# Kernel optimization log

Measured on AMD Instinct MI355X. Metric: run time of the kernel, lower is better.

## Reference

```python
import jax, jax.numpy as jnp
import numpy as np

B, S, IN, H, O, K = 64, 256, 512, 1024, 512, 4


def setup_inputs() -> dict:
    key = jax.random.key(0)
    ks = jax.random.split(key, 8)
    s = 1.0 / np.sqrt(H)  # torch RNNCell/Linear default uniform init bound
    return {
        "x_seq": jax.random.normal(ks[0], (B, S, IN), jnp.float32),
        "y_seq": jax.random.randint(ks[1], (B, S), 0, O, dtype=jnp.int64),
        "seq_mask": jnp.ones((B, S, 1), jnp.float32),
        "forced_num_ticks": K,
        "W_ih": jax.random.uniform(ks[2], (3 * H, IN), jnp.float32, -s, s),
        "W_hh": jax.random.uniform(ks[3], (3 * H, H), jnp.float32, -s, s),
        "b_ih": jax.random.uniform(ks[4], (3 * H,), jnp.float32, -s, s),
        "b_hh": jax.random.uniform(ks[5], (3 * H,), jnp.float32, -s, s),
        "W_fc": jax.random.uniform(ks[6], (O, H), jnp.float32, -s, s),
        "b_fc": jax.random.uniform(ks[7], (O,), jnp.float32, -s, s),
    }


def gru_cell(x, h, W_ih, W_hh, b_ih, b_hh):
    # torch.nn.GRUCell math
    gi = x @ W_ih.T + b_ih  # [B, 3H]
    gh = h @ W_hh.T + b_hh  # [B, 3H]
    i_r, i_z, i_n = jnp.split(gi, 3, axis=-1)
    h_r, h_z, h_n = jnp.split(gh, 3, axis=-1)
    r = jax.nn.sigmoid(i_r + h_r)
    z = jax.nn.sigmoid(i_z + h_z)
    n = jnp.tanh(i_n + r * h_n)
    return (1.0 - z) * n + z * h


def reference(x_seq, y_seq, seq_mask, forced_num_ticks, W_ih, W_hh, b_ih, b_hh, W_fc, b_fc):
    k = int(forced_num_ticks)
    b = x_seq.shape[0]
    # With forced_num_ticks=k, the inner while-loop runs exactly k ticks per
    # timestep for every sample; the same x_t / seq_mask[:,t,:] are reused
    # for all k ticks, and hidden state persists across timesteps.
    xs = jnp.repeat(x_seq, k, axis=1).transpose(1, 0, 2)      # [S*k, B, IN]
    sms = jnp.repeat(seq_mask, k, axis=1).transpose(1, 0, 2)  # [S*k, B, 1]
    h0 = jnp.zeros((b, W_hh.shape[1]), x_seq.dtype)

    def step(h, inp):
        x_t, sm_t = inp
        h_new = gru_cell(x_t, h, W_ih, W_hh, b_ih, b_hh)
        logits_t = (h_new @ W_fc.T + b_fc) * sm_t  # mask = not_finished * sm_t (not_finished always True)
        return h_new, logits_t

    _, logits = jax.lax.scan(step, h0, (xs, sms))  # logits: [S*k, B, O]
    logits_seq = logits.transpose(1, 0, 2)         # [B, S*k, O]
    y_res = jnp.repeat(y_seq, k, axis=1)           # [B, S*k]
    ok = jnp.repeat(seq_mask[:, :, 0] != 0, k, axis=1)  # [B, S*k] bool (mask_last=True)
    return logits_seq, y_res, ok
```

## Files before the change

### kernel.cpp

```cpp
#include <hip/hip_runtime.h>
#include <hip/hip_bf16.h>

#define B_ 64
#define S_ 256
#define IN_ 512
#define H_ 1024
#define O_ 512
#define K_ 4
#define T_ (S_*K_)
#define H3_ (3*H_)

#define NC_ 8
#define CPC_ 32
#define RPC_ 8

typedef __attribute__((ext_vector_type(8))) short bf16x8;
typedef __attribute__((ext_vector_type(4))) float f32x4;
typedef __attribute__((ext_vector_type(4))) unsigned int uint32x4;
typedef unsigned short ushort_t;
typedef unsigned int uint_t;
typedef unsigned long long ull_t;

__device__ __forceinline__ ushort_t f2b(float f) {
    union { float f; unsigned u; } v; v.f = f;
    unsigned r = v.u + 0x7FFFu + ((v.u >> 16) & 1u);
    return (ushort_t)(r >> 16);
}
__device__ __forceinline__ float b2f(ushort_t h) {
    union { unsigned u; float f; } v; v.u = ((unsigned)h) << 16; return v.f;
}

__global__ __launch_bounds__(256) void gi_gemm(const float* __restrict__ x,
                                               const float* __restrict__ Wih,
                                               const float* __restrict__ bih,
                                               ushort_t* __restrict__ gi) {
    const int NB = H3_ / 64;
    const int nb = blockIdx.x % NB;
    const int mb = blockIdx.x / NB;
    const int tid = threadIdx.x, lane = tid & 63, w = tid >> 6;
    const int wm = w >> 1, wn = w & 1;
    __shared__ ushort_t Al[64][40];
    __shared__ ushort_t Bl[64][40];
    f32x4 acc[2][2] = {};
    const int lrow = tid >> 2, lk = (tid & 3) * 8;
    for (int k0 = 0; k0 < IN_; k0 += 32) {
        const float* xs = &x[(size_t)(mb*64 + lrow)*IN_ + k0 + lk];
        const float* ws = &Wih[(size_t)(nb*64 + lrow)*IN_ + k0 + lk];
        #pragma unroll
        for (int i = 0; i < 8; ++i) Al[lrow][lk+i] = f2b(xs[i]);
        #pragma unroll
        for (int i = 0; i < 8; ++i) Bl[lrow][lk+i] = f2b(ws[i]);
        __syncthreads();
        const int fr = lane & 15, fk = (lane >> 4) * 8;
        #pragma unroll
        for (int mt = 0; mt < 2; ++mt) {
            bf16x8 a = *(const bf16x8*)&Al[wm*32 + mt*16 + fr][fk];
            #pragma unroll
            for (int nt = 0; nt < 2; ++nt) {
                bf16x8 b = *(const bf16x8*)&Bl[wn*32 + nt*16 + fr][fk];
                acc[mt][nt] = __builtin_amdgcn_mfma_f32_16x16x32_bf16(a, b, acc[mt][nt], 0, 0, 0);
            }
        }
        __syncthreads();
    }
    const int fr = lane & 15, fm = (lane >> 4) * 4;
    #pragma unroll
    for (int mt = 0; mt < 2; ++mt)
    #pragma unroll
    for (int nt = 0; nt < 2; ++nt)
    #pragma unroll
    for (int i = 0; i < 4; ++i) {
        int gm = mb*64 + wm*32 + mt*16 + fm + i;
        int gn = nb*64 + wn*32 + nt*16 + fr;
        gi[(size_t)gm*H3_ + gn] = f2b(acc[mt][nt][i] + bih[gn]);
    }
}

__global__ __launch_bounds__(256) void rec_kernel(const ushort_t* __restrict__ gi,
                                                  const float* __restrict__ Whh,
                                                  const float* __restrict__ bhh,
                                                  ushort_t* __restrict__ hstates,
                                                  ushort_t* __restrict__ xbuf,
                                                  int* __restrict__ flags) {
    const int bid = blockIdx.x;
    const int c  = bid & 7;
    const int cu = bid >> 3;
    const int tid = threadIdx.x, lane = tid & 63, w = tid >> 6;
    const int r_el = tid >> 5, jl = tid & 31;
    const int fr = lane & 15, koff8 = (lane >> 4) << 3;
    const int colbase = cu << 5;
    const int b0 = c * RPC_;

    __shared__ ushort_t wlds[48][1032];
    __shared__ float red[4][8][100];

    for (int e = tid * 4; e < 48 * 1024; e += 256 * 4) {
        int rr = e >> 10, k = e & 1023;
        int wrow = (rr < 32) ? (colbase + rr) : (H_ + colbase + (rr - 32));
        const float* src = &Whh[(size_t)wrow*H_ + k];
        #pragma unroll
        for (int i = 0; i < 4; ++i) wlds[rr][k + i] = f2b(src[i]);
    }
    bf16x8 bz1[8], bn0[8], bn1[8];
    #pragma unroll
    for (int ks = 0; ks < 8; ++ks) {
        const int kk = (w << 8) + (ks << 5) + koff8;
        const float* sz = &Whh[(size_t)(H_   + colbase + 16 + fr)*H_ + kk];
        const float* s0 = &Whh[(size_t)(2*H_ + colbase      + fr)*H_ + kk];
        const float* s1 = &Whh[(size_t)(2*H_ + colbase + 16 + fr)*H_ + kk];
        bf16x8 tz, t0, t1;
        #pragma unroll
        for (int i = 0; i < 8; ++i) {
            tz[i] = (short)f2b(sz[i]); t0[i] = (short)f2b(s0[i]); t1[i] = (short)f2b(s1[i]);
        }
        bz1[ks] = tz; bn0[ks] = t0; bn1[ks] = t1;
    }
    const float bh_r = bhh[colbase + jl];
    const float bh_z = bhh[H_ + colbase + jl];
    const float bh_n = bhh[2*H_ + colbase + jl];

    ushort_t g_r, g_z, g_n, p_r = 0, p_z = 0, p_n = 0;
    {
        size_t row = ((size_t)(b0 + r_el)*S_ + 0)*H3_ + colbase + jl;
        g_r = gi[row]; g_z = gi[row + H_]; g_n = gi[row + 2*H_];
    }
    float gir = 0.f, giz = 0.f, gin = 0.f;

    const char* xb_lane = (const char*)xbuf
        + ((size_t)c << 16)
        + (size_t)fr * 2048
        + (w << 9)
        + ((lane >> 4) << 4);

    float h_prev = 0.f;
    int* cflags = &flags[c << 5];
    __syncthreads();

    for (int t = 0; t < T_; ++t) {
        if ((t & 3) == 0) {
            if (t > 0) { g_r = p_r; g_z = p_z; g_n = p_n; }
            gir = b2f(g_r); giz = b2f(g_z); gin = b2f(g_n);
            int sn = (t >> 2) + 1; if (sn > S_ - 1) sn = S_ - 1;
            size_t row = ((size_t)(b0 + r_el)*S_ + sn)*H3_ + colbase + jl;
            p_r = gi[row]; p_z = gi[row + H_]; p_n = gi[row + 2*H_];
        }

        uint32x4 f0 = {}, f1 = {}, f2 = {}, f3 = {}, f4 = {}, f5 = {}, f6 = {}, f7 = {};
        if (t > 0) {
            const char* ab = xb_lane + (((size_t)((t - 1) & 1)) << 15);
            asm volatile(
                "global_load_dwordx4 %0, %8, off sc0 sc1\n\t"
                "global_load_dwordx4 %1, %8, off offset:64 sc0 sc1\n\t"
                "global_load_dwordx4 %2, %8, off offset:128 sc0 sc1\n\t"
                "global_load_dwordx4 %3, %8, off offset:192 sc0 sc1\n\t"
                "global_load_dwordx4 %4, %8, off offset:256 sc0 sc1\n\t"
                "global_load_dwordx4 %5, %8, off offset:320 sc0 sc1\n\t"
                "global_load_dwordx4 %6, %8, off offset:384 sc0 sc1\n\t"
                "global_load_dwordx4 %7, %8, off offset:448 sc0 sc1\n\t"
                "s_waitcnt vmcnt(0)"
                : "=&v"(f0), "=&v"(f1), "=&v"(f2), "=&v"(f3),
                  "=&v"(f4), "=&v"(f5), "=&v"(f6), "=&v"(f7)
                : "v"(ab)
                : "memory");
            __builtin_amdgcn_sched_barrier(0);
        }
        bf16x8 afr[8];
        afr[0] = *(bf16x8*)&f0; afr[1] = *(bf16x8*)&f1;
        afr[2] = *(bf16x8*)&f2; afr[3] = *(bf16x8*)&f3;
        afr[4] = *(bf16x8*)&f4; afr[5] = *(bf16x8*)&f5;
        afr[6] = *(bf16x8*)&f6; afr[7] = *(bf16x8*)&f7;

        f32x4 ar0 = {}, ar1 = {}, az0 = {}, az1 = {}, an0 = {}, an1 = {};
        #pragma unroll
        for (int ks = 0; ks < 8; ++ks) {
            const int k = (w << 8) + (ks << 5) + koff8;
            bf16x8 br0 = *(const bf16x8*)&wlds[fr][k];
            bf16x8 br1 = *(const bf16x8*)&wlds[16 + fr][k];
            bf16x8 bz0 = *(const bf16x8*)&wlds[32 + fr][k];
            ar0 = __builtin_amdgcn_mfma_f32_16x16x32_bf16(afr[ks], br0, ar0, 0, 0, 0);
            ar1 = __builtin_amdgcn_mfma_f32_16x16x32_bf16(afr[ks], br1, ar1, 0, 0, 0);
            az0 = __builtin_amdgcn_mfma_f32_16x16x32_bf16(afr[ks], bz0, az0, 0, 0, 0);
            az1 = __builtin_amdgcn_mfma_f32_16x16x32_bf16(afr[ks], bz1[ks], az1, 0, 0, 0);
            an0 = __builtin_amdgcn_mfma_f32_16x16x32_bf16(afr[ks], bn0[ks], an0, 0, 0, 0);
            an1 = __builtin_amdgcn_mfma_f32_16x16x32_bf16(afr[ks], bn1[ks], an1, 0, 0, 0);
        }
        if (lane < 32) {
            const int m = (lane >> 4) << 2, n = fr;
            #pragma unroll
            for (int i = 0; i < 4; ++i) {
                red[w][m+i][n]      = ar0[i];
                red[w][m+i][16+n]   = ar1[i];
                red[w][m+i][32+n]   = az0[i];
                red[w][m+i][48+n]   = az1[i];
                red[w][m+i][64+n]   = an0[i];
                red[w][m+i][80+n]   = an1[i];
            }
        }
        __syncthreads();

        float ghr = red[0][r_el][jl]    + red[1][r_el][jl]    + red[2][r_el][jl]    + red[3][r_el][jl];
        float ghz = red[0][r_el][32+jl] + red[1][r_el][32+jl] + red[2][r_el][32+jl] + red[3][r_el][32+jl];
        float ghn = red[0][r_el][64+jl] + red[1][r_el][64+jl] + red[2][r_el][64+jl] + red[3][r_el][64+jl];
        float rr_ = 1.f / (1.f + __expf(-(gir + ghr + bh_r)));
        float zz  = 1.f / (1.f + __expf(-(giz + ghz + bh_z)));
        float nn  = tanhf(gin + rr_ * (ghn + bh_n));
        float hn  = (1.f - zz) * nn + zz * h_prev;
        h_prev = hn;
        ushort_t hb = f2b(hn);

        hstates[((size_t)(b0 + r_el)*T_ + t)*H_ + colbase + jl] = hb;
        size_t xidx = ((size_t)c << 15) + ((size_t)(t & 1) << 14) + (r_el << 10) + colbase + jl;
        __hip_atomic_store(&xbuf[xidx], hb, __ATOMIC_RELAXED, __HIP_MEMORY_SCOPE_AGENT);

        __syncthreads();

        if (w == 0) {
            if (lane == 0)
                __hip_atomic_store(&cflags[cu], t + 1, __ATOMIC_RELAXED,
                                   __HIP_MEMORY_SCOPE_AGENT);
            for (;;) {
                int v = t + 1;
                if (lane < 32)
                    v = __hip_atomic_load(&cflags[lane], __ATOMIC_RELAXED,
                                          __HIP_MEMORY_SCOPE_AGENT);
                if (__all(v >= t + 1)) break;
                __builtin_amdgcn_s_sleep(1);
            }
        }
        __syncthreads();
    }
}

__global__ __launch_bounds__(256) void logits_gemm(const ushort_t* __restrict__ hstates,
                                                   const float* __restrict__ Wfc,
                                                   const float* __restrict__ bfc,
                                                   const float* __restrict__ sm,
                                                   float* __restrict__ out) {
    const int NB = O_ / 64;
    const int nb = blockIdx.x % NB;
    const int mb = blockIdx.x / NB;
    const int tid = threadIdx.x, lane = tid & 63, w = tid >> 6;
    const int wm = w >> 1, wn = w & 1;
    __shared__ ushort_t Al[64][40];
    __shared__ ushort_t Bl[64][40];
    f32x4 acc[2][2] = {};
    const int lrow = tid >> 2, lk = (tid & 3) * 8;
    for (int k0 = 0; k0 < H_; k0 += 32) {
        uint4 va = *(const uint4*)&hstates[(size_t)(mb*64 + lrow)*H_ + k0 + lk];
        *(uint4*)&Al[lrow][lk] = va;
        const float* ws = &Wfc[(size_t)(nb*64 + lrow)*H_ + k0 + lk];
        #pragma unroll
        for (int i = 0; i < 8; ++i) Bl[lrow][lk+i] = f2b(ws[i]);
        __syncthreads();
        const int fr = lane & 15, fk = (lane >> 4) * 8;
        #pragma unroll
        for (int mt = 0; mt < 2; ++mt) {
            bf16x8 a = *(const bf16x8*)&Al[wm*32 + mt*16 + fr][fk];
            #pragma unroll
            for (int nt = 0; nt < 2; ++nt) {
                bf16x8 b = *(const bf16x8*)&Bl[wn*32 + nt*16 + fr][fk];
                acc[mt][nt] = __builtin_amdgcn_mfma_f32_16x16x32_bf16(a, b, acc[mt][nt], 0, 0, 0);
            }
        }
        __syncthreads();
    }
    const int fr = lane & 15, fm = (lane >> 4) * 4;
    #pragma unroll
    for (int mt = 0; mt < 2; ++mt)
    #pragma unroll
    for (int nt = 0; nt < 2; ++nt)
    #pragma unroll
    for (int i = 0; i < 4; ++i) {
        int R  = mb*64 + wm*32 + mt*16 + fm + i;
        int gn = nb*64 + wn*32 + nt*16 + fr;
        int b  = R >> 10, t = R & (T_ - 1);
        float mval = sm[b*S_ + (t >> 2)];
        out[(size_t)R*O_ + gn] = (acc[mt][nt][i] + bfc[gn]) * mval;
    }
}

__global__ void tail_kernel(const int* __restrict__ y, const float* __restrict__ sm,
                            float* __restrict__ yout, float* __restrict__ okout) {
    int i = blockIdx.x * 256 + threadIdx.x;
    if (i < B_ * T_) {
        int b = i >> 10, t = i & 1023, s = t >> 2;
        yout[i]  = (float)y[b*S_ + s];
        okout[i] = (sm[b*S_ + s] != 0.0f) ? 1.0f : 0.0f;
    }
}

extern "C" void kernel_launch(void* const* d_in, const int* in_sizes, int n_in,
                              void* d_out, int out_size, void* d_ws, size_t ws_size,
                              hipStream_t stream) {
    (void)in_sizes; (void)n_in; (void)out_size; (void)ws_size;
    const float* x   = (const float*)d_in[0];
    const int*   y   = (const int*)d_in[1];
    const float* sm  = (const float*)d_in[2];
    const float* Wih = (const float*)d_in[4];
    const float* Whh = (const float*)d_in[5];
    const float* bih = (const float*)d_in[6];
    const float* bhh = (const float*)d_in[7];
    const float* Wfc = (const float*)d_in[8];
    const float* bfc = (const float*)d_in[9];

    char* ws = (char*)d_ws;
    ushort_t* gi      = (ushort_t*)ws;
    ushort_t* hstates = (ushort_t*)(ws + 100663296);
    ushort_t* xbuf    = (ushort_t*)(ws + 100663296 + 134217728);
    int*      flags   = (int*)(ws + 100663296 + 134217728 + 524288);

    hipMemsetAsync(flags, 0, 4096, stream);

    hipLaunchKernelGGL(gi_gemm, dim3((B_*S_/64)*(H3_/64)), dim3(256), 0, stream,
                       x, Wih, bih, gi);

    void* args[] = { (void*)&gi, (void*)&Whh, (void*)&bhh, (void*)&hstates,
                     (void*)&xbuf, (void*)&flags };
    hipLaunchCooperativeKernel((void*)rec_kernel, dim3(NC_*CPC_), dim3(256), args, 0, stream);

    hipLaunchKernelGGL(logits_gemm, dim3((B_*T_/64)*(O_/64)), dim3(256), 0, stream,
                       hstates, Wfc, bfc, sm, (float*)d_out);

    float* yout  = (float*)d_out + (size_t)B_*T_*O_;
    float* okout = yout + (size_t)B_*T_;
    hipLaunchKernelGGL(tail_kernel, dim3(B_*T_/256), dim3(256), 0, stream,
                       y, sm, yout, okout);
}
```

Baseline: 3.655 ms.

## Replace flag barrier with step-tagged hidden-state words polled directly

```diff
diff --git a/kernel.cpp b/kernel.cpp
--- a/kernel.cpp
+++ b/kernel.cpp
@@ -19,7 +19,6 @@
 typedef __attribute__((ext_vector_type(4))) unsigned int uint32x4;
 typedef unsigned short ushort_t;
 typedef unsigned int uint_t;
-typedef unsigned long long ull_t;
 
 __device__ __forceinline__ ushort_t f2b(float f) {
     union { float f; unsigned u; } v; v.f = f;
@@ -80,8 +79,7 @@
                                                   const float* __restrict__ Whh,
                                                   const float* __restrict__ bhh,
                                                   ushort_t* __restrict__ hstates,
-                                                  ushort_t* __restrict__ xbuf,
-                                                  int* __restrict__ flags) {
+                                                  uint_t* __restrict__ xbuf) {
     const int bid = blockIdx.x;
     const int c  = bid & 7;
     const int cu = bid >> 3;
@@ -92,7 +90,7 @@
     const int b0 = c * RPC_;
 
     __shared__ ushort_t wlds[48][1032];
-    __shared__ float red[4][8][100];
+    __shared__ float red[2][4][8][100];
 
     for (int e = tid * 4; e < 48 * 1024; e += 256 * 4) {
         int rr = e >> 10, k = e & 1023;
@@ -127,48 +125,74 @@
     float gir = 0.f, giz = 0.f, gin = 0.f;
 
     const char* xb_lane = (const char*)xbuf
-        + ((size_t)c << 16)
-        + (size_t)fr * 2048
-        + (w << 9)
-        + ((lane >> 4) << 4);
+        + ((size_t)c << 17)
+        + (size_t)fr * 4096
+        + (w << 10)
+        + ((lane >> 4) << 5);
 
     float h_prev = 0.f;
-    int* cflags = &flags[c << 5];
     __syncthreads();
 
     for (int t = 0; t < T_; ++t) {
         if ((t & 3) == 0) {
             if (t > 0) { g_r = p_r; g_z = p_z; g_n = p_n; }
             gir = b2f(g_r); giz = b2f(g_z); gin = b2f(g_n);
-            int sn = (t >> 2) + 1; if (sn > S_ - 1) sn = S_ - 1;
-            size_t row = ((size_t)(b0 + r_el)*S_ + sn)*H3_ + colbase + jl;
-            p_r = gi[row]; p_z = gi[row + H_]; p_n = gi[row + 2*H_];
-        }
-
-        uint32x4 f0 = {}, f1 = {}, f2 = {}, f3 = {}, f4 = {}, f5 = {}, f6 = {}, f7 = {};
+        }
+
+        uint32x4 f0={},f1={},f2={},f3={},f4={},f5={},f6={},f7={};
+        uint32x4 f8={},f9={},f10={},f11={},f12={},f13={},f14={},f15={};
         if (t > 0) {
-            const char* ab = xb_lane + (((size_t)((t - 1) & 1)) << 15);
-            asm volatile(
-                "global_load_dwordx4 %0, %8, off sc0 sc1\n\t"
-                "global_load_dwordx4 %1, %8, off offset:64 sc0 sc1\n\t"
-                "global_load_dwordx4 %2, %8, off offset:128 sc0 sc1\n\t"
-                "global_load_dwordx4 %3, %8, off offset:192 sc0 sc1\n\t"
-                "global_load_dwordx4 %4, %8, off offset:256 sc0 sc1\n\t"
-                "global_load_dwordx4 %5, %8, off offset:320 sc0 sc1\n\t"
-                "global_load_dwordx4 %6, %8, off offset:384 sc0 sc1\n\t"
-                "global_load_dwordx4 %7, %8, off offset:448 sc0 sc1\n\t"
-                "s_waitcnt vmcnt(0)"
-                : "=&v"(f0), "=&v"(f1), "=&v"(f2), "=&v"(f3),
-                  "=&v"(f4), "=&v"(f5), "=&v"(f6), "=&v"(f7)
-                : "v"(ab)
-                : "memory");
+            const char* ab = xb_lane + (((size_t)((t - 1) & 1)) << 16);
+            const uint_t tagw = ((uint_t)(t - 1)) << 16;
+            for (;;) {
+                asm volatile(
+                    "global_load_dwordx4 %0, %16, off sc0 sc1\n\t"
+                    "global_load_dwordx4 %1, %16, off offset:16 sc0 sc1\n\t"
+                    "global_load_dwordx4 %2, %16, off offset:128 sc0 sc1\n\t"
+                    "global_load_dwordx4 %3, %16, off offset:144 sc0 sc1\n\t"
+                    "global_load_dwordx4 %4, %16, off offset:256 sc0 sc1\n\t"
+                    "global_load_dwordx4 %5, %16, off offset:272 sc0 sc1\n\t"
+                    "global_load_dwordx4 %6, %16, off offset:384 sc0 sc1\n\t"
+                    "global_load_dwordx4 %7, %16, off offset:400 sc0 sc1\n\t"
+                    "global_load_dwordx4 %8, %16, off offset:512 sc0 sc1\n\t"
+                    "global_load_dwordx4 %9, %16, off offset:528 sc0 sc1\n\t"
+                    "global_load_dwordx4 %10, %16, off offset:640 sc0 sc1\n\t"
+                    "global_load_dwordx4 %11, %16, off offset:656 sc0 sc1\n\t"
+                    "global_load_dwordx4 %12, %16, off offset:768 sc0 sc1\n\t"
+                    "global_load_dwordx4 %13, %16, off offset:784 sc0 sc1\n\t"
+                    "global_load_dwordx4 %14, %16, off offset:896 sc0 sc1\n\t"
+                    "global_load_dwordx4 %15, %16, off offset:912 sc0 sc1\n\t"
+                    "s_waitcnt vmcnt(0)"
+                    : "=&v"(f0), "=&v"(f1), "=&v"(f2), "=&v"(f3),
+                      "=&v"(f4), "=&v"(f5), "=&v"(f6), "=&v"(f7),
+                      "=&v"(f8), "=&v"(f9), "=&v"(f10), "=&v"(f11),
+                      "=&v"(f12), "=&v"(f13), "=&v"(f14), "=&v"(f15)
+                    : "v"(ab)
+                    : "memory");
+                uint_t acc = 0;
+                #define ACC4(F) acc |= (F[0]^tagw); acc |= (F[1]^tagw); \
+                                acc |= (F[2]^tagw); acc |= (F[3]^tagw);
+                ACC4(f0) ACC4(f1) ACC4(f2) ACC4(f3) ACC4(f4) ACC4(f5) ACC4(f6) ACC4(f7)
+                ACC4(f8) ACC4(f9) ACC4(f10) ACC4(f11) ACC4(f12) ACC4(f13) ACC4(f14) ACC4(f15)
+                #undef ACC4
+                if (__all((fr >= 8) || ((acc & 0xFFFF0000u) == 0u))) break;
+            }
             __builtin_amdgcn_sched_barrier(0);
         }
         bf16x8 afr[8];
-        afr[0] = *(bf16x8*)&f0; afr[1] = *(bf16x8*)&f1;
-        afr[2] = *(bf16x8*)&f2; afr[3] = *(bf16x8*)&f3;
-        afr[4] = *(bf16x8*)&f4; afr[5] = *(bf16x8*)&f5;
-        afr[6] = *(bf16x8*)&f6; afr[7] = *(bf16x8*)&f7;
+        {
+            union U { uint_t u[4]; bf16x8 v; };
+            #define PK(DST, A, B) { U x_; \
+                x_.u[0] = (A[0] & 0xffffu) | (A[1] << 16); \
+                x_.u[1] = (A[2] & 0xffffu) | (A[3] << 16); \
+                x_.u[2] = (B[0] & 0xffffu) | (B[1] << 16); \
+                x_.u[3] = (B[2] & 0xffffu) | (B[3] << 16); DST = x_.v; }
+            PK(afr[0], f0, f1)   PK(afr[1], f2, f3)
+            PK(afr[2], f4, f5)   PK(afr[3], f6, f7)
+            PK(afr[4], f8, f9)   PK(afr[5], f10, f11)
+            PK(afr[6], f12, f13) PK(afr[7], f14, f15)
+            #undef PK
+        }
 
         f32x4 ar0 = {}, ar1 = {}, az0 = {}, az1 = {}, an0 = {}, an1 = {};
         #pragma unroll
@@ -184,50 +208,48 @@
             an0 = __builtin_amdgcn_mfma_f32_16x16x32_bf16(afr[ks], bn0[ks], an0, 0, 0, 0);
             an1 = __builtin_amdgcn_mfma_f32_16x16x32_bf16(afr[ks], bn1[ks], an1, 0, 0, 0);
         }
-        if (lane < 32) {
-            const int m = (lane >> 4) << 2, n = fr;
-            #pragma unroll
-            for (int i = 0; i < 4; ++i) {
-                red[w][m+i][n]      = ar0[i];
-                red[w][m+i][16+n]   = ar1[i];
-                red[w][m+i][32+n]   = az0[i];
-                red[w][m+i][48+n]   = az1[i];
-                red[w][m+i][64+n]   = an0[i];
-                red[w][m+i][80+n]   = an1[i];
+        {
+            const int par = t & 1;
+            if (lane < 32) {
+                const int m = (lane >> 4) << 2, n = fr;
+                #pragma unroll
+                for (int i = 0; i < 4; ++i) {
+                    red[par][w][m+i][n]      = ar0[i];
+                    red[par][w][m+i][16+n]   = ar1[i];
+                    red[par][w][m+i][32+n]   = az0[i];
+                    red[par][w][m+i][48+n]   = az1[i];
+                    red[par][w][m+i][64+n]   = an0[i];
+                    red[par][w][m+i][80+n]   = an1[i];
+                }
             }
         }
         __syncthreads();
 
-        float ghr = red[0][r_el][jl]    + red[1][r_el][jl]    + red[2][r_el][jl]    + red[3][r_el][jl];
-        float ghz = red[0][r_el][32+jl] + red[1][r_el][32+jl] + red[2][r_el][32+jl] + red[3][r_el][32+jl];
-        float ghn = red[0][r_el][64+jl] + red[1][r_el][64+jl] + red[2][r_el][64+jl] + red[3][r_el][64+jl];
-        float rr_ = 1.f / (1.f + __expf(-(gir + ghr + bh_r)));
-        float zz  = 1.f / (1.f + __expf(-(giz + ghz + bh_z)));
-        float nn  = tanhf(gin + rr_ * (ghn + bh_n));
+        const int par = t & 1;
+        float ghr = red[par][0][r_el][jl]    + red[par][1][r_el][jl]    + red[par][2][r_el][jl]    + red[par][3][r_el][jl];
+        float ghz = red[par][0][r_el][32+jl] + red[par][1][r_el][32+jl] + red[par][2][r_el][32+jl] + red[par][3][r_el][32+jl];
+        float ghn = red[par][0][r_el][64+jl] + red[par][1][r_el][64+jl] + red[par][2][r_el][64+jl] + red[par][3][r_el][64+jl];
+        float rr_ = __builtin_amdgcn_rcpf(1.f + __expf(-(gir + ghr + bh_r)));
+        float zz  = __builtin_amdgcn_rcpf(1.f + __expf(-(giz + ghz + bh_z)));
+        float xx  = gin + rr_ * (ghn + bh_n);
+        xx = fminf(fmaxf(xx, -15.f), 15.f);
+        float e2  = __expf(2.f * xx);
+        float nn  = (e2 - 1.f) * __builtin_amdgcn_rcpf(e2 + 1.f);
         float hn  = (1.f - zz) * nn + zz * h_prev;
         h_prev = hn;
         ushort_t hb = f2b(hn);
 
+        uint_t word = (((uint_t)t) << 16) | (uint_t)hb;
+        size_t xidx = ((size_t)c << 15) + ((size_t)(t & 1) << 14) + (r_el << 10) + colbase + jl;
+        __hip_atomic_store(&xbuf[xidx], word, __ATOMIC_RELAXED, __HIP_MEMORY_SCOPE_AGENT);
+
         hstates[((size_t)(b0 + r_el)*T_ + t)*H_ + colbase + jl] = hb;
-        size_t xidx = ((size_t)c << 15) + ((size_t)(t & 1) << 14) + (r_el << 10) + colbase + jl;
-        __hip_atomic_store(&xbuf[xidx], hb, __ATOMIC_RELAXED, __HIP_MEMORY_SCOPE_AGENT);
-
-        __syncthreads();
-
-        if (w == 0) {
-            if (lane == 0)
-                __hip_atomic_store(&cflags[cu], t + 1, __ATOMIC_RELAXED,
-                                   __HIP_MEMORY_SCOPE_AGENT);
-            for (;;) {
-                int v = t + 1;
-                if (lane < 32)
-                    v = __hip_atomic_load(&cflags[lane], __ATOMIC_RELAXED,
-                                          __HIP_MEMORY_SCOPE_AGENT);
-                if (__all(v >= t + 1)) break;
-                __builtin_amdgcn_s_sleep(1);
-            }
-        }
-        __syncthreads();
+
+        if ((t & 3) == 0) {
+            int sn = (t >> 2) + 1; if (sn > S_ - 1) sn = S_ - 1;
+            size_t row = ((size_t)(b0 + r_el)*S_ + sn)*H3_ + colbase + jl;
+            p_r = gi[row]; p_z = gi[row + H_]; p_n = gi[row + 2*H_];
+        }
     }
 }
 
@@ -306,16 +328,13 @@
     char* ws = (char*)d_ws;
     ushort_t* gi      = (ushort_t*)ws;
     ushort_t* hstates = (ushort_t*)(ws + 100663296);
-    ushort_t* xbuf    = (ushort_t*)(ws + 100663296 + 134217728);
-    int*      flags   = (int*)(ws + 100663296 + 134217728 + 524288);
-
-    hipMemsetAsync(flags, 0, 4096, stream);
+    uint_t*   xbuf    = (uint_t*)(ws + 100663296 + 134217728);
 
     hipLaunchKernelGGL(gi_gemm, dim3((B_*S_/64)*(H3_/64)), dim3(256), 0, stream,
                        x, Wih, bih, gi);
 
     void* args[] = { (void*)&gi, (void*)&Whh, (void*)&bhh, (void*)&hstates,
-                     (void*)&xbuf, (void*)&flags };
+                     (void*)&xbuf };
     hipLaunchCooperativeKernel((void*)rec_kernel, dim3(NC_*CPC_), dim3(256), args, 0, stream);
 
     hipLaunchKernelGGL(logits_gemm, dim3((B_*T_/64)*(O_/64)), dim3(256), 0, stream,
```

Measured after the change: 4.562 ms. 1.25x slower.
